# Optimization experiments

Hardware: AMD Instinct MI355X
Metric: run time of the kernel (lower is better)

## Reference

```python
import jax, jax.numpy as jnp
import numpy as np

HID = 1152      # vision_hidden_size
HEADS = 16      # vision_num_heads
HD = HID // HEADS  # 72
INTER = 4304    # vision_intermediate_size
SEQ = 16384     # total vision tokens
WIN = 64        # tokens per attention window
EPS = 1e-6


def setup_inputs() -> dict:
    key = jax.random.key(0)
    ks = jax.random.split(key, 14)
    f32 = jnp.float32
    x = jax.random.normal(ks[0], (SEQ, HID), f32)
    # RoPE tables: standard rotary angles, full head_dim via concat(ang, ang)
    inv_freq = 1.0 / (10000.0 ** (jnp.arange(0, HD // 2, dtype=f32) / (HD // 2)))
    ang = jnp.arange(SEQ, dtype=f32)[:, None] * inv_freq[None, :]
    emb = jnp.concatenate([ang, ang], axis=-1)          # [SEQ, HD]
    cos, sin = jnp.cos(emb), jnp.sin(emb)
    cu_seqlens = jnp.arange(SEQ // WIN + 1, dtype=jnp.int32) * WIN  # uniform windows
    sc = 0.02
    return {
        "x": x, "cos": cos, "sin": sin, "cu_seqlens": cu_seqlens,
        "qkv_w": jax.random.normal(ks[1], (HID, 3 * HID), f32) * sc,
        "qkv_b": jnp.zeros((3 * HID,), f32),
        "proj_w": jax.random.normal(ks[2], (HID, HID), f32) * sc,
        "proj_b": jnp.zeros((HID,), f32),
        "ln1_w": jnp.ones((HID,), f32), "ln1_b": jnp.zeros((HID,), f32),
        "ln2_w": jnp.ones((HID,), f32), "ln2_b": jnp.zeros((HID,), f32),
        "fc1_w": jax.random.normal(ks[3], (HID, INTER), f32) * sc,
        "fc1_b": jnp.zeros((INTER,), f32),
        "fc2_w": jax.random.normal(ks[4], (INTER, HID), f32) * sc,
        "fc2_b": jnp.zeros((HID,), f32),
    }


def _layer_norm(h, w, b):
    hf = h.astype(jnp.float32)
    mean = jnp.mean(hf, axis=-1, keepdims=True)
    var = jnp.mean((hf - mean) ** 2, axis=-1, keepdims=True)
    return ((hf - mean) * jax.lax.rsqrt(var + EPS)) * w + b


def _rotate_half(t):
    t1, t2 = jnp.split(t, 2, axis=-1)
    return jnp.concatenate((-t2, t1), axis=-1)


def reference(x, cos, sin, cu_seqlens,
              qkv_w, qkv_b, proj_w, proj_b,
              ln1_w, ln1_b, ln2_w, ln2_b,
              fc1_w, fc1_b, fc2_w, fc2_b):
    S = x.shape[0]
    n_win = cu_seqlens.shape[0] - 1
    W = S // n_win  # uniform windows (block-diagonal attention)

    # --- attention branch ---
    h = _layer_norm(x, ln1_w, ln1_b)
    qkv = h @ qkv_w + qkv_b
    q, k, v = jnp.split(qkv, 3, axis=-1)
    q = q.reshape(S, HEADS, HD)
    k = k.reshape(S, HEADS, HD)
    v = v.reshape(S, HEADS, HD)
    c = cos[:, None, :HD]
    s = sin[:, None, :HD]
    q = q * c + _rotate_half(q) * s
    k = k * c + _rotate_half(k) * s
    # block-diagonal windowed attention: [n_win, W, HEADS, HD]
    qw = q.reshape(n_win, W, HEADS, HD).astype(jnp.float32)
    kw = k.reshape(n_win, W, HEADS, HD).astype(jnp.float32)
    vw = v.reshape(n_win, W, HEADS, HD).astype(jnp.float32)
    scores = jnp.einsum('wqhd,wkhd->whqk', qw, kw) * (HD ** -0.5)
    probs = jax.nn.softmax(scores, axis=-1)
    out = jnp.einsum('whqk,wkhd->wqhd', probs, vw).reshape(S, HID)
    x = x + (out @ proj_w + proj_b)

    # --- MLP branch ---
    h2 = _layer_norm(x, ln2_w, ln2_b)
    m = jax.nn.gelu(h2 @ fc1_w + fc1_b, approximate=True)
    return x + (m @ fc2_w + fc2_b)
```

## Files before the change

### kernel.cpp

```cpp
#include <hip/hip_runtime.h>
#include <stdint.h>


#define SEQ   16384
#define HID   1152
#define NH    16
#define HDIM  72
#define INTER 4304
#define INTERP 4352
#define QKVN  3456

using bf16x8 = __attribute__((ext_vector_type(8))) __bf16;
using f32x4  = __attribute__((ext_vector_type(4))) float;

__device__ __forceinline__ float bf2f(uint16_t u){ return __uint_as_float(((uint32_t)u)<<16); }
__device__ __forceinline__ uint16_t f2bf(float f){
  uint32_t u = __float_as_uint(f);
  u += 0x7fffu + ((u>>16)&1u);
  return (uint16_t)(u>>16);
}
__device__ __forceinline__ float gelu_tanh(float x){
  float t = tanhf(0.7978845608028654f*(x + 0.044715f*x*x*x));
  return 0.5f*x*(1.0f + t);
}
__device__ __forceinline__ void async_load16(const void* g, void* l){
  __builtin_amdgcn_global_load_lds((__attribute__((address_space(1))) void*)(void*)g,
                                   (__attribute__((address_space(3))) void*)l, 16, 0, 0);
}

__global__ void transpose_cast(const float* __restrict__ src, uint16_t* __restrict__ dst,
                               int R, int C, int Rp)
{
  __shared__ float tile[32][33];
  const int tx = threadIdx.x & 31, ty = threadIdx.x >> 5;
  const int c = blockIdx.x*32 + tx;
  #pragma unroll
  for (int s = 0; s < 4; ++s){
    const int r = blockIdx.y*32 + ty + s*8;
    tile[ty + s*8][tx] = (r < R && c < C) ? src[(size_t)r*C + c] : 0.0f;
  }
  __syncthreads();
  #pragma unroll
  for (int s = 0; s < 4; ++s){
    const int oc = blockIdx.x*32 + ty + s*8;
    const int orr = blockIdx.y*32 + tx;
    dst[(size_t)oc*Rp + orr] = f2bf(tile[tx][ty + s*8]);
  }
}

__global__ void ln_kernel(const float* __restrict__ x, const float* __restrict__ w,
                          const float* __restrict__ b, uint16_t* __restrict__ out)
{
  const int wid = threadIdx.x >> 6, lane = threadIdx.x & 63;
  const int row = blockIdx.x*4 + wid;
  const float* xr = x + (size_t)row*HID;
  float v[18];
  float s = 0.f;
  #pragma unroll
  for (int t = 0; t < 18; ++t){ v[t] = xr[lane + t*64]; s += v[t]; }
  #pragma unroll
  for (int m = 32; m; m >>= 1) s += __shfl_xor(s, m, 64);
  const float mean = s * (1.0f/HID);
  float q = 0.f;
  #pragma unroll
  for (int t = 0; t < 18; ++t){ float d = v[t]-mean; q += d*d; }
  #pragma unroll
  for (int m = 32; m; m >>= 1) q += __shfl_xor(q, m, 64);
  const float rstd = rsqrtf(q*(1.0f/HID) + 1e-6f);
  uint16_t* orow = out + (size_t)row*HID;
  #pragma unroll
  for (int t = 0; t < 18; ++t){
    const int j = lane + t*64;
    orow[j] = f2bf((v[t]-mean)*rstd*w[j] + b[j]);
  }
}

__global__ void rope_kernel(uint16_t* __restrict__ qkv, const float* __restrict__ cosb,
                            const float* __restrict__ sinb)
{
  const int idx = blockIdx.x*256 + threadIdx.x;
  const int s  = idx / (NH*36);
  const int r1 = idx - s*(NH*36);
  const int h  = r1 / 36;
  const int d  = r1 - h*36;
  const float c  = cosb[s*HDIM + d];
  const float sn = sinb[s*HDIM + d];
  const size_t b = (size_t)s*QKVN + h*HDIM + d;
  float q1 = bf2f(qkv[b]), q2 = bf2f(qkv[b+36]);
  qkv[b]    = f2bf(q1*c - q2*sn);
  qkv[b+36] = f2bf(q2*c + q1*sn);
  float k1 = bf2f(qkv[b+HID]), k2 = bf2f(qkv[b+HID+36]);
  qkv[b+HID]    = f2bf(k1*c - k2*sn);
  qkv[b+HID+36] = f2bf(k2*c + k1*sn);
}

__global__ __launch_bounds__(256,2) void attn_kernel(const uint16_t* __restrict__ qkv,
                                                     uint16_t* __restrict__ outb)
{
  __shared__ float Q[64*76];
  __shared__ float K[64*76];
  __shared__ float V[64*76];
  __shared__ float P[64*68];
  const int tid = threadIdx.x;
  const int win = blockIdx.x >> 4, h = blockIdx.x & 15;
  const size_t base = (size_t)win*64*QKVN + h*HDIM;
  {
    const int r = tid >> 2, q4 = tid & 3;
    const size_t rb = base + (size_t)r*QKVN;
    #pragma unroll
    for (int p0 = 0; p0 < 9; ++p0){
      const int p = q4*9 + p0;
      const uint32_t uq = *(const uint32_t*)(qkv + rb + 2*p);
      const uint32_t uk = *(const uint32_t*)(qkv + rb + HID + 2*p);
      const uint32_t uv = *(const uint32_t*)(qkv + rb + 2*HID + 2*p);
      Q[r*76+2*p] = bf2f((uint16_t)uq); Q[r*76+2*p+1] = bf2f((uint16_t)(uq>>16));
      K[r*76+2*p] = bf2f((uint16_t)uk); K[r*76+2*p+1] = bf2f((uint16_t)(uk>>16));
      V[r*76+2*p] = bf2f((uint16_t)uv); V[r*76+2*p+1] = bf2f((uint16_t)(uv>>16));
    }
  }
  __syncthreads();
  const int rg = tid >> 4, cg = tid & 15;
  const int r0 = rg*4, c0 = cg*4;
  float sc[4][4] = {};
  #pragma unroll 3
  for (int kk = 0; kk < 18; ++kk){
    float4 qv[4], kv[4];
    #pragma unroll
    for (int i = 0; i < 4; ++i) qv[i] = *(const float4*)&Q[(r0+i)*76 + kk*4];
    #pragma unroll
    for (int j = 0; j < 4; ++j) kv[j] = *(const float4*)&K[(c0+j)*76 + kk*4];
    #pragma unroll
    for (int i = 0; i < 4; ++i)
      #pragma unroll
      for (int j = 0; j < 4; ++j)
        sc[i][j] += qv[i].x*kv[j].x + qv[i].y*kv[j].y + qv[i].z*kv[j].z + qv[i].w*kv[j].w;
  }
  const float scale = 0.11785113019775793f;
  #pragma unroll
  for (int i = 0; i < 4; ++i){
    float a0 = sc[i][0]*scale, a1 = sc[i][1]*scale, a2 = sc[i][2]*scale, a3 = sc[i][3]*scale;
    float m = fmaxf(fmaxf(a0,a1), fmaxf(a2,a3));
    m = fmaxf(m, __shfl_xor(m, 1, 16));
    m = fmaxf(m, __shfl_xor(m, 2, 16));
    m = fmaxf(m, __shfl_xor(m, 4, 16));
    m = fmaxf(m, __shfl_xor(m, 8, 16));
    float e0 = __expf(a0-m), e1 = __expf(a1-m), e2 = __expf(a2-m), e3 = __expf(a3-m);
    float sm = e0+e1+e2+e3;
    sm += __shfl_xor(sm, 1, 16);
    sm += __shfl_xor(sm, 2, 16);
    sm += __shfl_xor(sm, 4, 16);
    sm += __shfl_xor(sm, 8, 16);
    const float inv = 1.0f/sm;
    *(float4*)&P[(r0+i)*68 + c0] = make_float4(e0*inv, e1*inv, e2*inv, e3*inv);
  }
  __syncthreads();
  for (int d4 = cg; d4 < 18; d4 += 16){
    float4 o[4] = {};
    #pragma unroll 4
    for (int k4 = 0; k4 < 16; ++k4){
      float4 pr[4];
      #pragma unroll
      for (int i = 0; i < 4; ++i) pr[i] = *(const float4*)&P[(r0+i)*68 + k4*4];
      const float4 v0 = *(const float4*)&V[(k4*4+0)*76 + d4*4];
      const float4 v1 = *(const float4*)&V[(k4*4+1)*76 + d4*4];
      const float4 v2 = *(const float4*)&V[(k4*4+2)*76 + d4*4];
      const float4 v3 = *(const float4*)&V[(k4*4+3)*76 + d4*4];
      #pragma unroll
      for (int i = 0; i < 4; ++i){
        o[i].x += pr[i].x*v0.x + pr[i].y*v1.x + pr[i].z*v2.x + pr[i].w*v3.x;
        o[i].y += pr[i].x*v0.y + pr[i].y*v1.y + pr[i].z*v2.y + pr[i].w*v3.y;
        o[i].z += pr[i].x*v0.z + pr[i].y*v1.z + pr[i].z*v2.z + pr[i].w*v3.z;
        o[i].w += pr[i].x*v0.w + pr[i].y*v1.w + pr[i].z*v2.w + pr[i].w*v3.w;
      }
    }
    #pragma unroll
    for (int i = 0; i < 4; ++i){
      const int token = win*64 + r0 + i;
      const size_t ob = (size_t)token*HID + h*HDIM + d4*4;
      outb[ob+0] = f2bf(o[i].x); outb[ob+1] = f2bf(o[i].y);
      outb[ob+2] = f2bf(o[i].z); outb[ob+3] = f2bf(o[i].w);
    }
  }
}

template<int EPI>
__global__ __launch_bounds__(256,3) void gemm_bt(
    const uint16_t* __restrict__ A, const uint16_t* __restrict__ Bt,
    const float* __restrict__ bias, int Nb,
    const float* res, void* outp, int N, int K, int NB)
{
  __shared__ uint16_t sA[128*64];
  __shared__ uint16_t sB[128*64];
  const int tid = threadIdx.x, wid = tid >> 6, lane = tid & 63;
  const int per  = gridDim.x >> 3;
  const int tile = (blockIdx.x & 7)*per + (blockIdx.x >> 3);
  const int mb   = tile / NB;
  const int mBase = mb*128, nBase = (tile - mb*NB)*128;
  const int wm = wid >> 1, wn = wid & 1;
  const int sr = lane >> 2;
  const int sk = lane & 3;
  const int gk = sk ^ ((sr >> 1) & 3);
  const int rr = lane & 15;
  const int rq = lane >> 4;
  const int rp = rq ^ ((rr >> 1) & 3);
  f32x4 acc[4][4] = {};

  for (int k0 = 0; k0 < K; k0 += 64){
    __syncthreads();
    #pragma unroll
    for (int j = 0; j < 4; ++j){
      const int c  = wid*4 + j;
      const int rc = c >> 1, h = c & 1;
      const size_t gcol = (size_t)(k0 + h*32 + gk*8);
      async_load16(A  + (size_t)(mBase + rc*16 + sr)*K + gcol, &sA[c*512]);
      async_load16(Bt + (size_t)(nBase + rc*16 + sr)*K + gcol, &sB[c*512]);
    }
    __syncthreads();
    #pragma unroll
    for (int h = 0; h < 2; ++h){
      bf16x8 af[4], bfr[4];
      #pragma unroll
      for (int i = 0; i < 4; ++i)
        af[i] = *(const bf16x8*)&sA[((wm*4 + i)*2 + h)*512 + rr*32 + rp*8];
      #pragma unroll
      for (int j = 0; j < 4; ++j)
        bfr[j] = *(const bf16x8*)&sB[((wn*4 + j)*2 + h)*512 + rr*32 + rp*8];
      #pragma unroll
      for (int i = 0; i < 4; ++i)
        #pragma unroll
        for (int j = 0; j < 4; ++j)
          acc[i][j] = __builtin_amdgcn_mfma_f32_16x16x32_bf16(af[i], bfr[j], acc[i][j], 0, 0, 0);
    }
  }

  const int rqd = (lane>>4)*4, cl = lane & 15;
  #pragma unroll
  for (int i = 0; i < 4; ++i){
    #pragma unroll
    for (int j = 0; j < 4; ++j){
      const int col = nBase + wn*64 + j*16 + cl;
      const float bv = (col < Nb) ? bias[col] : 0.0f;
      #pragma unroll
      for (int r = 0; r < 4; ++r){
        const int row = mBase + wm*64 + i*16 + rqd + r;
        const float v = acc[i][j][r] + bv;
        const size_t o = (size_t)row*N + col;
        if (EPI == 0)      ((uint16_t*)outp)[o] = f2bf(v);
        else if (EPI == 1) ((uint16_t*)outp)[o] = f2bf(gelu_tanh(v));
        else               ((float*)outp)[o] = v + res[o];
      }
    }
  }
}

extern "C" void kernel_launch(void* const* d_in, const int* in_sizes, int n_in,
                              void* d_out, int out_size, void* d_ws, size_t ws_size,
                              hipStream_t stream)
{
  const float* x      = (const float*)d_in[0];
  const float* cosb   = (const float*)d_in[1];
  const float* sinb   = (const float*)d_in[2];
  const float* qkv_w  = (const float*)d_in[4];
  const float* qkv_b  = (const float*)d_in[5];
  const float* proj_w = (const float*)d_in[6];
  const float* proj_b = (const float*)d_in[7];
  const float* ln1_w  = (const float*)d_in[8];
  const float* ln1_b  = (const float*)d_in[9];
  const float* ln2_w  = (const float*)d_in[10];
  const float* ln2_b  = (const float*)d_in[11];
  const float* fc1_w  = (const float*)d_in[12];
  const float* fc1_b  = (const float*)d_in[13];
  const float* fc2_w  = (const float*)d_in[14];
  const float* fc2_b  = (const float*)d_in[15];

  char* ws = (char*)d_ws;
  uint16_t* Wqkv  = (uint16_t*)(ws + 0);
  uint16_t* Wproj = (uint16_t*)(ws + 7962624);
  uint16_t* Wfc1  = (uint16_t*)(ws + 10616832);
  uint16_t* Wfc2  = (uint16_t*)(ws + 20643840);
  uint16_t* Hbuf  = (uint16_t*)(ws + 30670848);
  uint16_t* QKV   = (uint16_t*)(ws + 68419584);
  uint16_t* MB    = QKV;
  float* X1 = (float*)d_out;

  transpose_cast<<<dim3(108,36), 256, 0, stream>>>(qkv_w, Wqkv, 1152, 3456, 1152);
  transpose_cast<<<dim3(36,36),  256, 0, stream>>>(proj_w, Wproj, 1152, 1152, 1152);
  transpose_cast<<<dim3(136,36), 256, 0, stream>>>(fc1_w, Wfc1, 1152, 4304, 1152);
  transpose_cast<<<dim3(36,136), 256, 0, stream>>>(fc2_w, Wfc2, 4304, 1152, 4352);

  ln_kernel<<<4096, 256, 0, stream>>>(x, ln1_w, ln1_b, Hbuf);
  gemm_bt<0><<<27*128, 256, 0, stream>>>(Hbuf, Wqkv, qkv_b, QKVN, nullptr, QKV, QKVN, HID, 27);
  rope_kernel<<<36864, 256, 0, stream>>>(QKV, cosb, sinb);
  attn_kernel<<<4096, 256, 0, stream>>>(QKV, Hbuf);
  gemm_bt<2><<<9*128, 256, 0, stream>>>(Hbuf, Wproj, proj_b, HID, x, X1, HID, HID, 9);
  ln_kernel<<<4096, 256, 0, stream>>>(X1, ln2_w, ln2_b, Hbuf);
  gemm_bt<1><<<34*128, 256, 0, stream>>>(Hbuf, Wfc1, fc1_b, INTER, nullptr, MB, INTERP, HID, 34);
  gemm_bt<2><<<9*128, 256, 0, stream>>>(MB, Wfc2, fc2_b, HID, X1, X1, HID, INTERP, 9);
}
```

Measured before the change: 1.175 ms.

## Use 256x128 GEMM tiles with 512 threads and a triple-buffered async LDS pipeline

The bf16 GEMM moves from 128x128 tiles with 256 threads to 256x128 tiles with 512 threads (8 waves). Global-to-LDS loads go through a three-slot ring buffer, staged in two halves interleaved with the MFMA phases, with explicit vmcnt waits and raw s_barrier calls in place of the two __syncthreads per k-step. It also raises wave priority around the MFMA blocks. The aim is to hide global load latency, cut barrier cost and increase reuse of B per tile, at the price of 144KB of LDS per block, fragile hand-counted waitcnt values, and fewer blocks for the narrow N=1152 GEMMs.

```diff
diff --git a/kernel.cpp b/kernel.cpp
--- a/kernel.cpp
+++ b/kernel.cpp
@@ -184,53 +184,105 @@
 }
 
 template<int EPI>
-__global__ __launch_bounds__(256,3) void gemm_bt(
+__global__ __launch_bounds__(512,2) void gemm_bt(
     const uint16_t* __restrict__ A, const uint16_t* __restrict__ Bt,
     const float* __restrict__ bias, int Nb,
     const float* res, void* outp, int N, int K, int NB)
 {
-  __shared__ uint16_t sA[128*64];
-  __shared__ uint16_t sB[128*64];
+  __shared__ uint16_t sM[3*24576];
   const int tid = threadIdx.x, wid = tid >> 6, lane = tid & 63;
   const int per  = gridDim.x >> 3;
   const int tile = (blockIdx.x & 7)*per + (blockIdx.x >> 3);
   const int mb   = tile / NB;
-  const int mBase = mb*128, nBase = (tile - mb*NB)*128;
+  const int mBase = mb*256, nBase = (tile - mb*NB)*128;
   const int wm = wid >> 1, wn = wid & 1;
-  const int sr = lane >> 2;
-  const int sk = lane & 3;
-  const int gk = sk ^ ((sr >> 1) & 3);
-  const int rr = lane & 15;
-  const int rq = lane >> 4;
-  const int rp = rq ^ ((rr >> 1) & 3);
+  const int sr = lane >> 2, sk = lane & 3, gk = sk ^ ((sr >> 1) & 3);
+  const int rr = lane & 15, rq = lane >> 4, rp = rq ^ ((rr >> 1) & 3);
+
+  const uint16_t* pA0; const uint16_t* pA1; const uint16_t* pA2; const uint16_t* pA3;
+  const uint16_t* pB0; const uint16_t* pB1;
+  {
+    const int cA0 = wid*4+0, cA1 = wid*4+1, cA2 = wid*4+2, cA3 = wid*4+3;
+    pA0 = A + (size_t)(mBase + (cA0>>1)*16 + sr)*K + (cA0&1)*32 + gk*8;
+    pA1 = A + (size_t)(mBase + (cA1>>1)*16 + sr)*K + (cA1&1)*32 + gk*8;
+    pA2 = A + (size_t)(mBase + (cA2>>1)*16 + sr)*K + (cA2&1)*32 + gk*8;
+    pA3 = A + (size_t)(mBase + (cA3>>1)*16 + sr)*K + (cA3&1)*32 + gk*8;
+    const int cB0 = wid*2+0, cB1 = wid*2+1;
+    pB0 = Bt + (size_t)(nBase + (cB0>>1)*16 + sr)*K + (cB0&1)*32 + gk*8;
+    pB1 = Bt + (size_t)(nBase + (cB1>>1)*16 + sr)*K + (cB1&1)*32 + gk*8;
+  }
+  const int NT = K >> 6;
   f32x4 acc[4][4] = {};
 
-  for (int k0 = 0; k0 < K; k0 += 64){
-    __syncthreads();
-    #pragma unroll
-    for (int j = 0; j < 4; ++j){
-      const int c  = wid*4 + j;
-      const int rc = c >> 1, h = c & 1;
-      const size_t gcol = (size_t)(k0 + h*32 + gk*8);
-      async_load16(A  + (size_t)(mBase + rc*16 + sr)*K + gcol, &sA[c*512]);
-      async_load16(Bt + (size_t)(nBase + rc*16 + sr)*K + gcol, &sB[c*512]);
-    }
-    __syncthreads();
-    #pragma unroll
-    for (int h = 0; h < 2; ++h){
+  auto stageP1 = [&](int slot){
+    uint16_t* sl = &sM[slot*24576];
+    async_load16(pA0, &sl[(wid*4+0)*512]);
+    async_load16(pA1, &sl[(wid*4+1)*512]);
+    async_load16(pB0, &sl[16384 + (wid*2+0)*512]);
+  };
+  auto stageP2 = [&](int slot){
+    uint16_t* sl = &sM[slot*24576];
+    async_load16(pA2, &sl[(wid*4+2)*512]);
+    async_load16(pA3, &sl[(wid*4+3)*512]);
+    async_load16(pB1, &sl[16384 + (wid*2+1)*512]);
+  };
+  auto advance = [&](){ pA0+=64; pA1+=64; pA2+=64; pA3+=64; pB0+=64; pB1+=64; };
+
+  stageP1(0); stageP2(0); advance();
+  stageP1(1); stageP2(1); advance();
+
+  int cs = 0;
+  for (int t = 0; t < NT; ++t){
+    const int ss = (cs >= 1) ? cs - 1 : cs + 2;
+    if (t + 2 < NT){
+      stageP1(ss);
+      asm volatile("s_waitcnt vmcnt(9)" ::: "memory");
+    } else if (t + 1 < NT){
+      asm volatile("s_waitcnt vmcnt(6)" ::: "memory");
+    } else {
+      asm volatile("s_waitcnt vmcnt(0)" ::: "memory");
+    }
+    __builtin_amdgcn_s_barrier();
+    asm volatile("" ::: "memory");
+    const uint16_t* sl = &sM[cs*24576];
+    {
       bf16x8 af[4], bfr[4];
       #pragma unroll
       for (int i = 0; i < 4; ++i)
-        af[i] = *(const bf16x8*)&sA[((wm*4 + i)*2 + h)*512 + rr*32 + rp*8];
+        af[i] = *(const bf16x8*)&sl[((wm*4+i)*2+0)*512 + rr*32 + rp*8];
       #pragma unroll
       for (int j = 0; j < 4; ++j)
-        bfr[j] = *(const bf16x8*)&sB[((wn*4 + j)*2 + h)*512 + rr*32 + rp*8];
+        bfr[j] = *(const bf16x8*)&sl[16384 + ((wn*4+j)*2+0)*512 + rr*32 + rp*8];
+      __builtin_amdgcn_s_setprio(1);
       #pragma unroll
       for (int i = 0; i < 4; ++i)
         #pragma unroll
         for (int j = 0; j < 4; ++j)
           acc[i][j] = __builtin_amdgcn_mfma_f32_16x16x32_bf16(af[i], bfr[j], acc[i][j], 0, 0, 0);
-    }
+      __builtin_amdgcn_s_setprio(0);
+    }
+    if (t + 2 < NT) stageP2(ss);
+    {
+      bf16x8 af[4], bfr[4];
+      #pragma unroll
+      for (int i = 0; i < 4; ++i)
+        af[i] = *(const bf16x8*)&sl[((wm*4+i)*2+1)*512 + rr*32 + rp*8];
+      #pragma unroll
+      for (int j = 0; j < 4; ++j)
+        bfr[j] = *(const bf16x8*)&sl[16384 + ((wn*4+j)*2+1)*512 + rr*32 + rp*8];
+      __builtin_amdgcn_s_setprio(1);
+      #pragma unroll
+      for (int i = 0; i < 4; ++i)
+        #pragma unroll
+        for (int j = 0; j < 4; ++j)
+          acc[i][j] = __builtin_amdgcn_mfma_f32_16x16x32_bf16(af[i], bfr[j], acc[i][j], 0, 0, 0);
+      __builtin_amdgcn_s_setprio(0);
+    }
+    advance();
+    asm volatile("s_waitcnt lgkmcnt(0)" ::: "memory");
+    __builtin_amdgcn_s_barrier();
+    asm volatile("" ::: "memory");
+    cs = (cs + 1 == 3) ? 0 : cs + 1;
   }
 
   const int rqd = (lane>>4)*4, cl = lane & 15;
@@ -289,11 +341,11 @@
   transpose_cast<<<dim3(36,136), 256, 0, stream>>>(fc2_w, Wfc2, 4304, 1152, 4352);
 
   ln_kernel<<<4096, 256, 0, stream>>>(x, ln1_w, ln1_b, Hbuf);
-  gemm_bt<0><<<27*128, 256, 0, stream>>>(Hbuf, Wqkv, qkv_b, QKVN, nullptr, QKV, QKVN, HID, 27);
+  gemm_bt<0><<<64*27, 512, 0, stream>>>(Hbuf, Wqkv, qkv_b, QKVN, nullptr, QKV, QKVN, HID, 27);
   rope_kernel<<<36864, 256, 0, stream>>>(QKV, cosb, sinb);
   attn_kernel<<<4096, 256, 0, stream>>>(QKV, Hbuf);
-  gemm_bt<2><<<9*128, 256, 0, stream>>>(Hbuf, Wproj, proj_b, HID, x, X1, HID, HID, 9);
+  gemm_bt<2><<<64*9, 512, 0, stream>>>(Hbuf, Wproj, proj_b, HID, x, X1, HID, HID, 9);
   ln_kernel<<<4096, 256, 0, stream>>>(X1, ln2_w, ln2_b, Hbuf);
-  gemm_bt<1><<<34*128, 256, 0, stream>>>(Hbuf, Wfc1, fc1_b, INTER, nullptr, MB, INTERP, HID, 34);
-  gemm_bt<2><<<9*128, 256, 0, stream>>>(MB, Wfc2, fc2_b, HID, X1, X1, HID, INTERP, 9);
-}
+  gemm_bt<1><<<64*34, 512, 0, stream>>>(Hbuf, Wfc1, fc1_b, INTER, nullptr, MB, INTERP, HID, 34);
+  gemm_bt<2><<<64*9, 512, 0, stream>>>(MB, Wfc2, fc2_b, HID, X1, X1, HID, INTERP, 9);
+}
```

Result: no change. 1.173 ms (-0.2%).

## Rewrite GEMM as 256x256 tile, 8-wave, double-buffered LDS pipeline

Applied to the files above, without the earlier changes.

Replaces the 128x128, 4-wave GEMM with a 256x256 tile computed by 8 waves. LDS is double-buffered so global-to-LDS async loads for the next K step overlap the MFMA work, interleaved in quarter steps with barriers and s_setprio. Weight buffers are padded to multiples of 256 with an Nout guard on stores. The aim is higher data reuse per tile and hidden load latency, at the cost of more registers and LDS, lower occupancy, and padded wasted compute on the N edges.

```diff
diff --git a/kernel.cpp b/kernel.cpp
--- a/kernel.cpp
+++ b/kernel.cpp
@@ -184,70 +184,131 @@
 }
 
 template<int EPI>
-__global__ __launch_bounds__(256,3) void gemm_bt(
+__global__ __launch_bounds__(512,2) void gemm_bt(
     const uint16_t* __restrict__ A, const uint16_t* __restrict__ Bt,
     const float* __restrict__ bias, int Nb,
-    const float* res, void* outp, int N, int K, int NB)
-{
-  __shared__ uint16_t sA[128*64];
-  __shared__ uint16_t sB[128*64];
+    const float* res, void* outp, int N, int Nout, int K, int NB)
+{
+  __shared__ uint16_t sM[2*32768];
   const int tid = threadIdx.x, wid = tid >> 6, lane = tid & 63;
   const int per  = gridDim.x >> 3;
   const int tile = (blockIdx.x & 7)*per + (blockIdx.x >> 3);
   const int mb   = tile / NB;
-  const int mBase = mb*128, nBase = (tile - mb*NB)*128;
-  const int wm = wid >> 1, wn = wid & 1;
-  const int sr = lane >> 2;
-  const int sk = lane & 3;
-  const int gk = sk ^ ((sr >> 1) & 3);
-  const int rr = lane & 15;
-  const int rq = lane >> 4;
-  const int rp = rq ^ ((rr >> 1) & 3);
-  f32x4 acc[4][4] = {};
-
-  for (int k0 = 0; k0 < K; k0 += 64){
-    __syncthreads();
-    #pragma unroll
-    for (int j = 0; j < 4; ++j){
-      const int c  = wid*4 + j;
-      const int rc = c >> 1, h = c & 1;
-      const size_t gcol = (size_t)(k0 + h*32 + gk*8);
-      async_load16(A  + (size_t)(mBase + rc*16 + sr)*K + gcol, &sA[c*512]);
-      async_load16(Bt + (size_t)(nBase + rc*16 + sr)*K + gcol, &sB[c*512]);
-    }
-    __syncthreads();
-    #pragma unroll
-    for (int h = 0; h < 2; ++h){
-      bf16x8 af[4], bfr[4];
-      #pragma unroll
-      for (int i = 0; i < 4; ++i)
-        af[i] = *(const bf16x8*)&sA[((wm*4 + i)*2 + h)*512 + rr*32 + rp*8];
-      #pragma unroll
-      for (int j = 0; j < 4; ++j)
-        bfr[j] = *(const bf16x8*)&sB[((wn*4 + j)*2 + h)*512 + rr*32 + rp*8];
-      #pragma unroll
-      for (int i = 0; i < 4; ++i)
-        #pragma unroll
-        for (int j = 0; j < 4; ++j)
-          acc[i][j] = __builtin_amdgcn_mfma_f32_16x16x32_bf16(af[i], bfr[j], acc[i][j], 0, 0, 0);
-    }
+  const int mBase = mb*256, nBase = (tile - mb*NB)*256;
+  const int wm = wid >> 2, wn = wid & 3;
+  const int sr = lane >> 2, sk = lane & 3, gk = sk ^ ((sr >> 1) & 3);
+  const int rr = lane & 15, rq = lane >> 4, rp = rq ^ ((rr >> 1) & 3);
+
+  const uint16_t* pA0 = A  + (size_t)(mBase + (wid*2+0)*16 + sr)*K + gk*8;
+  const uint16_t* pA1 = A  + (size_t)(mBase + (wid*2+1)*16 + sr)*K + gk*8;
+  const uint16_t* pB0 = Bt + (size_t)(nBase + (wid*2+0)*16 + sr)*K + gk*8;
+  const uint16_t* pB1 = Bt + (size_t)(nBase + (wid*2+1)*16 + sr)*K + gk*8;
+  const int c0 = (wid*2+0)*2, c1 = (wid*2+1)*2;
+
+  auto stageA = [&](int b, int h, int koff){
+    uint16_t* sl = &sM[b*32768];
+    async_load16(pA0 + koff + h*32, &sl[(c0+h)*512]);
+    async_load16(pA1 + koff + h*32, &sl[(c1+h)*512]);
+  };
+  auto stageB = [&](int b, int h, int koff){
+    uint16_t* sl = &sM[b*32768 + 16384];
+    async_load16(pB0 + koff + h*32, &sl[(c0+h)*512]);
+    async_load16(pB1 + koff + h*32, &sl[(c1+h)*512]);
+  };
+
+  const int NT = K >> 6;
+  f32x4 acc[8][4] = {};
+
+  stageA(0,0,0); stageB(0,0,0); stageA(0,1,0); stageB(0,1,0);
+  asm volatile("s_waitcnt vmcnt(4)" ::: "memory");
+  __builtin_amdgcn_s_barrier();
+
+  int k0 = 64;
+  const int aB = wm*8;
+  for (int t = 0; t < NT; ++t){
+    const uint16_t* sl = &sM[(t&1)*32768];
+    const int nb2 = (t&1)^1;
+    const bool pf = (t+1 < NT);
+    bf16x8 af[4], bfr[4];
+    #pragma unroll
+    for (int i=0;i<4;++i) af[i]  = *(const bf16x8*)&sl[((aB+i)*2+0)*512 + rr*32 + rp*8];
+    #pragma unroll
+    for (int j=0;j<4;++j) bfr[j] = *(const bf16x8*)&sl[16384 + ((wn*4+j)*2+0)*512 + rr*32 + rp*8];
+    if (pf) stageA(nb2, 0, k0);
+    __builtin_amdgcn_s_barrier();
+    asm volatile("s_waitcnt lgkmcnt(0)" ::: "memory");
+    __builtin_amdgcn_s_setprio(1);
+    #pragma unroll
+    for (int i=0;i<4;++i)
+      #pragma unroll
+      for (int j=0;j<4;++j)
+        acc[i][j] = __builtin_amdgcn_mfma_f32_16x16x32_bf16(af[i], bfr[j], acc[i][j], 0, 0, 0);
+    __builtin_amdgcn_s_setprio(0);
+    __builtin_amdgcn_s_barrier();
+    #pragma unroll
+    for (int i=0;i<4;++i) af[i]  = *(const bf16x8*)&sl[((aB+4+i)*2+0)*512 + rr*32 + rp*8];
+    if (pf){ stageB(nb2, 0, k0);
+             asm volatile("s_waitcnt vmcnt(4)" ::: "memory"); }
+    else   { asm volatile("s_waitcnt vmcnt(0)" ::: "memory"); }
+    __builtin_amdgcn_s_barrier();
+    asm volatile("s_waitcnt lgkmcnt(0)" ::: "memory");
+    __builtin_amdgcn_s_setprio(1);
+    #pragma unroll
+    for (int i=0;i<4;++i)
+      #pragma unroll
+      for (int j=0;j<4;++j)
+        acc[4+i][j] = __builtin_amdgcn_mfma_f32_16x16x32_bf16(af[i], bfr[j], acc[4+i][j], 0, 0, 0);
+    __builtin_amdgcn_s_setprio(0);
+    __builtin_amdgcn_s_barrier();
+    #pragma unroll
+    for (int i=0;i<4;++i) af[i]  = *(const bf16x8*)&sl[((aB+i)*2+1)*512 + rr*32 + rp*8];
+    #pragma unroll
+    for (int j=0;j<4;++j) bfr[j] = *(const bf16x8*)&sl[16384 + ((wn*4+j)*2+1)*512 + rr*32 + rp*8];
+    if (pf) stageA(nb2, 1, k0);
+    __builtin_amdgcn_s_barrier();
+    asm volatile("s_waitcnt lgkmcnt(0)" ::: "memory");
+    __builtin_amdgcn_s_setprio(1);
+    #pragma unroll
+    for (int i=0;i<4;++i)
+      #pragma unroll
+      for (int j=0;j<4;++j)
+        acc[i][j] = __builtin_amdgcn_mfma_f32_16x16x32_bf16(af[i], bfr[j], acc[i][j], 0, 0, 0);
+    __builtin_amdgcn_s_setprio(0);
+    __builtin_amdgcn_s_barrier();
+    #pragma unroll
+    for (int i=0;i<4;++i) af[i]  = *(const bf16x8*)&sl[((aB+4+i)*2+1)*512 + rr*32 + rp*8];
+    if (pf){ stageB(nb2, 1, k0);
+             asm volatile("s_waitcnt vmcnt(4)" ::: "memory"); }
+    __builtin_amdgcn_s_barrier();
+    asm volatile("s_waitcnt lgkmcnt(0)" ::: "memory");
+    __builtin_amdgcn_s_setprio(1);
+    #pragma unroll
+    for (int i=0;i<4;++i)
+      #pragma unroll
+      for (int j=0;j<4;++j)
+        acc[4+i][j] = __builtin_amdgcn_mfma_f32_16x16x32_bf16(af[i], bfr[j], acc[4+i][j], 0, 0, 0);
+    __builtin_amdgcn_s_setprio(0);
+    __builtin_amdgcn_s_barrier();
+    k0 += 64;
   }
 
   const int rqd = (lane>>4)*4, cl = lane & 15;
   #pragma unroll
-  for (int i = 0; i < 4; ++i){
+  for (int i8 = 0; i8 < 8; ++i8){
     #pragma unroll
     for (int j = 0; j < 4; ++j){
       const int col = nBase + wn*64 + j*16 + cl;
-      const float bv = (col < Nb) ? bias[col] : 0.0f;
-      #pragma unroll
-      for (int r = 0; r < 4; ++r){
-        const int row = mBase + wm*64 + i*16 + rqd + r;
-        const float v = acc[i][j][r] + bv;
-        const size_t o = (size_t)row*N + col;
-        if (EPI == 0)      ((uint16_t*)outp)[o] = f2bf(v);
-        else if (EPI == 1) ((uint16_t*)outp)[o] = f2bf(gelu_tanh(v));
-        else               ((float*)outp)[o] = v + res[o];
+      if (col < Nout){
+        const float bv = (col < Nb) ? bias[col] : 0.0f;
+        #pragma unroll
+        for (int r = 0; r < 4; ++r){
+          const int row = mBase + wm*128 + i8*16 + rqd + r;
+          const float v = acc[i8][j][r] + bv;
+          const size_t o = (size_t)row*N + col;
+          if (EPI == 0)      ((uint16_t*)outp)[o] = f2bf(v);
+          else if (EPI == 1) ((uint16_t*)outp)[o] = f2bf(gelu_tanh(v));
+          else               ((float*)outp)[o] = v + res[o];
+        }
       }
     }
   }
@@ -275,25 +336,25 @@
 
   char* ws = (char*)d_ws;
   uint16_t* Wqkv  = (uint16_t*)(ws + 0);
-  uint16_t* Wproj = (uint16_t*)(ws + 7962624);
-  uint16_t* Wfc1  = (uint16_t*)(ws + 10616832);
-  uint16_t* Wfc2  = (uint16_t*)(ws + 20643840);
-  uint16_t* Hbuf  = (uint16_t*)(ws + 30670848);
-  uint16_t* QKV   = (uint16_t*)(ws + 68419584);
+  uint16_t* Wproj = (uint16_t*)(ws + 8257536);
+  uint16_t* Wfc1  = (uint16_t*)(ws + 11206656);
+  uint16_t* Wfc2  = (uint16_t*)(ws + 21233664);
+  uint16_t* Hbuf  = (uint16_t*)(ws + 32374784);
+  uint16_t* QKV   = (uint16_t*)(ws + 70123520);
   uint16_t* MB    = QKV;
   float* X1 = (float*)d_out;
 
-  transpose_cast<<<dim3(108,36), 256, 0, stream>>>(qkv_w, Wqkv, 1152, 3456, 1152);
-  transpose_cast<<<dim3(36,36),  256, 0, stream>>>(proj_w, Wproj, 1152, 1152, 1152);
+  transpose_cast<<<dim3(112,36), 256, 0, stream>>>(qkv_w, Wqkv, 1152, 3456, 1152);
+  transpose_cast<<<dim3(40,36),  256, 0, stream>>>(proj_w, Wproj, 1152, 1152, 1152);
   transpose_cast<<<dim3(136,36), 256, 0, stream>>>(fc1_w, Wfc1, 1152, 4304, 1152);
-  transpose_cast<<<dim3(36,136), 256, 0, stream>>>(fc2_w, Wfc2, 4304, 1152, 4352);
+  transpose_cast<<<dim3(40,136), 256, 0, stream>>>(fc2_w, Wfc2, 4304, 1152, 4352);
 
   ln_kernel<<<4096, 256, 0, stream>>>(x, ln1_w, ln1_b, Hbuf);
-  gemm_bt<0><<<27*128, 256, 0, stream>>>(Hbuf, Wqkv, qkv_b, QKVN, nullptr, QKV, QKVN, HID, 27);
+  gemm_bt<0><<<64*14, 512, 0, stream>>>(Hbuf, Wqkv, qkv_b, QKVN, nullptr, QKV, QKVN, QKVN, HID, 14);
   rope_kernel<<<36864, 256, 0, stream>>>(QKV, cosb, sinb);
   attn_kernel<<<4096, 256, 0, stream>>>(QKV, Hbuf);
-  gemm_bt<2><<<9*128, 256, 0, stream>>>(Hbuf, Wproj, proj_b, HID, x, X1, HID, HID, 9);
+  gemm_bt<2><<<64*5, 512, 0, stream>>>(Hbuf, Wproj, proj_b, HID, x, X1, HID, HID, HID, 5);
   ln_kernel<<<4096, 256, 0, stream>>>(X1, ln2_w, ln2_b, Hbuf);
-  gemm_bt<1><<<34*128, 256, 0, stream>>>(Hbuf, Wfc1, fc1_b, INTER, nullptr, MB, INTERP, HID, 34);
-  gemm_bt<2><<<9*128, 256, 0, stream>>>(MB, Wfc2, fc2_b, HID, X1, X1, HID, INTERP, 9);
-}
+  gemm_bt<1><<<64*17, 512, 0, stream>>>(Hbuf, Wfc1, fc1_b, INTER, nullptr, MB, INTERP, INTERP, HID, 17);
+  gemm_bt<2><<<64*5, 512, 0, stream>>>(MB, Wfc2, fc2_b, HID, X1, X1, HID, HID, INTERP, 5);
+}
```

New measurement: 1.344 ms. 14.3% more time.
